# Optimization experiments

Hardware: AMD Instinct MI355X
Metric: run time of the kernel (lower is better)

The kernel has to match this reference:

```python
import jax, jax.numpy as jnp
from jax import lax
import numpy as np

UNITS = 128
IN_DIM = 512
BATCH = 128
SEQ = 1024


def setup_inputs() -> dict:
    key = jax.random.key(0)
    k1, k2, k3 = jax.random.split(key, 3)
    x = jax.random.normal(k1, (BATCH, SEQ, IN_DIM), dtype=jnp.float32)
    # glorot-ish scaling for stability
    W = jax.random.normal(k2, (IN_DIM, 4 * UNITS), dtype=jnp.float32) * (1.0 / np.sqrt(IN_DIM))
    U = jax.random.normal(k3, (UNITS, 4 * UNITS), dtype=jnp.float32) * (1.0 / np.sqrt(UNITS))
    b = jnp.zeros((4 * UNITS,), dtype=jnp.float32)
    return {"x": x, "W": W, "U": U, "b": b}


def reference(x, W, U, b):
    # Keras LSTM with activation='tanh' AND recurrent_activation='tanh'
    # (all four gates use tanh, unlike the standard sigmoid gates).
    # Gate order in Keras kernels: i, f, g(cell candidate), o.
    B = x.shape[0]
    units = U.shape[0]
    # Precompute input projections for all timesteps: [T, B, 4*units]
    xW = jnp.einsum('bti,ij->tbj', x, W) + b

    def step(carry, xw_t):
        h, c = carry
        z = xw_t + h @ U  # [B, 4*units]
        i, f, g, o = jnp.split(z, 4, axis=-1)
        i = jnp.tanh(i)
        f = jnp.tanh(f)
        g = jnp.tanh(g)
        o = jnp.tanh(o)
        c_new = f * c + i * g
        h_new = o * jnp.tanh(c_new)
        return (h_new, c_new), None

    h0 = jnp.zeros((B, units), dtype=x.dtype)
    c0 = jnp.zeros((B, units), dtype=x.dtype)
    (h_last, _), _ = lax.scan(step, (h0, c0), xW)
    return h_last  # [B, units] (return_sequences=False)
```

## Files before the change

### kernel.cpp

```cpp
#include <hip/hip_runtime.h>
#include <hip/hip_bf16.h>


#define UNITS 128
#define IN_DIM 512
#define BATCH 128
#define SEQ 1024
#define GATES 512
#define M_ROWS (BATCH * SEQ)

typedef __attribute__((ext_vector_type(8))) short short8;
typedef __attribute__((ext_vector_type(4))) float floatx4;

__device__ __forceinline__ unsigned short f2bf(float f) {
    unsigned int x = __builtin_bit_cast(unsigned int, f);
    unsigned int r = (x + 0x7fffu + ((x >> 16) & 1u)) >> 16;
    return (unsigned short)r;
}
__device__ __forceinline__ float bf2f(unsigned short u) {
    unsigned int x = ((unsigned int)u) << 16;
    return __builtin_bit_cast(float, x);
}
__device__ __forceinline__ unsigned int pack2(float lo, float hi) {
    return (unsigned int)f2bf(lo) | ((unsigned int)f2bf(hi) << 16);
}

__device__ __forceinline__ float fast_tanh(float x) {
    float xc = fminf(12.0f, fmaxf(-12.0f, x));
    float e = __expf(2.0f * xc);
    return 1.0f - 2.0f * __builtin_amdgcn_rcpf(e + 1.0f);
}

__global__ void k_wt(const float* __restrict__ W, unsigned short* __restrict__ Wt) {
    int idx = blockIdx.x * 256 + threadIdx.x;
    int n = idx >> 9;
    int k = idx & 511;
    Wt[idx] = f2bf(W[k * 512 + n]);
}

template <bool XWF32>
__global__ void __launch_bounds__(256, 2)
k_gemm(const float* __restrict__ A, const unsigned short* __restrict__ Bt,
       void* __restrict__ Cout) {
    __shared__ __align__(16) unsigned short As[128 * 40];
    __shared__ __align__(16) unsigned short Bs[128 * 40];
    const int tid = threadIdx.x;
    const int m0 = blockIdx.y << 7;
    const int n0 = blockIdx.x << 7;
    const int l = tid & 63;
    const int w = tid >> 6;
    const int wr = (w >> 1) << 6;
    const int wc = (w & 1) << 6;
    const int lrow = l & 15;
    const int lq = l >> 4;

    floatx4 acc[4][4] = {};

    const int srow = tid >> 1;
    const int soff = (tid & 1) << 4;
    const float* ap = A + (size_t)(m0 + srow) * 512 + soff;
    const unsigned short* bp = Bt + (size_t)(n0 + srow) * 512 + soff;
    unsigned short* as = &As[srow * 40 + soff];
    unsigned short* bs = &Bs[srow * 40 + soff];

    for (int k0 = 0; k0 < 512; k0 += 32) {
        float4 a0 = *(const float4*)(ap + k0);
        float4 a1 = *(const float4*)(ap + k0 + 4);
        float4 a2 = *(const float4*)(ap + k0 + 8);
        float4 a3 = *(const float4*)(ap + k0 + 12);
        uint4 b0 = *(const uint4*)(bp + k0);
        uint4 b1 = *(const uint4*)(bp + k0 + 8);
        __syncthreads();
        uint4 pa0, pa1;
        pa0.x = pack2(a0.x, a0.y); pa0.y = pack2(a0.z, a0.w);
        pa0.z = pack2(a1.x, a1.y); pa0.w = pack2(a1.z, a1.w);
        pa1.x = pack2(a2.x, a2.y); pa1.y = pack2(a2.z, a2.w);
        pa1.z = pack2(a3.x, a3.y); pa1.w = pack2(a3.z, a3.w);
        *(uint4*)as = pa0;
        *(uint4*)(as + 8) = pa1;
        *(uint4*)bs = b0;
        *(uint4*)(bs + 8) = b1;
        __syncthreads();
        short8 af[4], bfv[4];
#pragma unroll
        for (int mi = 0; mi < 4; ++mi)
            af[mi] = *(const short8*)&As[(wr + mi * 16 + lrow) * 40 + lq * 8];
#pragma unroll
        for (int ni = 0; ni < 4; ++ni)
            bfv[ni] = *(const short8*)&Bs[(wc + ni * 16 + lrow) * 40 + lq * 8];
#pragma unroll
        for (int mi = 0; mi < 4; ++mi)
#pragma unroll
            for (int ni = 0; ni < 4; ++ni)
                acc[mi][ni] = __builtin_amdgcn_mfma_f32_16x16x32_bf16(
                    af[mi], bfv[ni], acc[mi][ni], 0, 0, 0);
    }
#pragma unroll
    for (int mi = 0; mi < 4; ++mi) {
#pragma unroll
        for (int ni = 0; ni < 4; ++ni) {
            int row = m0 + wr + mi * 16 + lq * 4;
            int col = n0 + wc + ni * 16 + lrow;
            if (XWF32) {
                float* Cf = (float*)Cout;
#pragma unroll
                for (int r = 0; r < 4; ++r)
                    Cf[(size_t)(row + r) * 512 + col] = acc[mi][ni][r];
            } else {
                unsigned short* Cb = (unsigned short*)Cout;
#pragma unroll
                for (int r = 0; r < 4; ++r)
                    Cb[(size_t)(row + r) * 512 + col] = f2bf(acc[mi][ni][r]);
            }
        }
    }
}

template <bool XWF32>
__global__ void __launch_bounds__(512, 2)
k_scan(const void* __restrict__ xwv, const float* __restrict__ U,
       const float* __restrict__ bias, float* __restrict__ out) {
    __shared__ __align__(16) float hbuf[2 * 160];
    const int j = threadIdx.x;
    const int bb = blockIdx.x;
    const int m = j >> 2;
    const int r = j & 3;

    float u0[32], u1[32], u2[32], u3[32];
#pragma unroll
    for (int kk = 0; kk < 32; ++kk) {
        const float* Up = U + (size_t)(r * 32 + kk) * 512 + m;
        u0[kk] = Up[0];
        u1[kk] = Up[128];
        u2[kk] = Up[256];
        u3[kk] = Up[384];
    }
    const float bj = bias[r * 128 + m];

    if (j < 160) hbuf[j] = 0.0f;
    __syncthreads();

    const float* xwf = (const float*)xwv + (size_t)bb * SEQ * 512 + r * 128 + m;
    const unsigned short* xwb =
        (const unsigned short*)xwv + (size_t)bb * SEQ * 512 + r * 128 + m;

    float c = 0.0f, hval = 0.0f;
    float xw_cur = XWF32 ? xwf[0] : bf2f(xwb[0]);
    for (int t = 0; t < SEQ; ++t) {
        float xw_next = 0.0f;
        if (t + 1 < SEQ)
            xw_next = XWF32 ? xwf[(size_t)(t + 1) * 512]
                            : bf2f(xwb[(size_t)(t + 1) * 512]);

        const float xb = xw_cur + bj;
        float a0 = (r == 0) ? xb : 0.0f;
        float a1 = (r == 1) ? xb : 0.0f;
        float a2 = (r == 2) ? xb : 0.0f;
        float a3 = (r == 3) ? xb : 0.0f;

        const float4* h4 =
            (const float4*)(hbuf + (t & 1) * 160 + r * 40);
#pragma unroll
        for (int i = 0; i < 8; ++i) {
            float4 hv = h4[i];
            a0 = fmaf(hv.x, u0[4 * i + 0], a0);
            a1 = fmaf(hv.x, u1[4 * i + 0], a1);
            a2 = fmaf(hv.x, u2[4 * i + 0], a2);
            a3 = fmaf(hv.x, u3[4 * i + 0], a3);
            a0 = fmaf(hv.y, u0[4 * i + 1], a0);
            a1 = fmaf(hv.y, u1[4 * i + 1], a1);
            a2 = fmaf(hv.y, u2[4 * i + 1], a2);
            a3 = fmaf(hv.y, u3[4 * i + 1], a3);
            a0 = fmaf(hv.z, u0[4 * i + 2], a0);
            a1 = fmaf(hv.z, u1[4 * i + 2], a1);
            a2 = fmaf(hv.z, u2[4 * i + 2], a2);
            a3 = fmaf(hv.z, u3[4 * i + 2], a3);
            a0 = fmaf(hv.w, u0[4 * i + 3], a0);
            a1 = fmaf(hv.w, u1[4 * i + 3], a1);
            a2 = fmaf(hv.w, u2[4 * i + 3], a2);
            a3 = fmaf(hv.w, u3[4 * i + 3], a3);
        }
        a0 += __shfl_xor(a0, 1);
        a1 += __shfl_xor(a1, 1);
        a2 += __shfl_xor(a2, 1);
        a3 += __shfl_xor(a3, 1);
        a0 += __shfl_xor(a0, 2);
        a1 += __shfl_xor(a1, 2);
        a2 += __shfl_xor(a2, 2);
        a3 += __shfl_xor(a3, 2);

        const float gi = fast_tanh(a0);
        const float gf = fast_tanh(a1);
        const float gg = fast_tanh(a2);
        const float go = fast_tanh(a3);
        c = fmaf(gf, c, gi * gg);
        hval = go * fast_tanh(c);

        if (r == 0)
            hbuf[((t + 1) & 1) * 160 + (m >> 5) * 40 + (m & 31)] = hval;
        __syncthreads();
        xw_cur = xw_next;
    }
    if (r == 0) out[bb * UNITS + m] = hval;
}

extern "C" void kernel_launch(void* const* d_in, const int* in_sizes, int n_in,
                              void* d_out, int out_size, void* d_ws, size_t ws_size,
                              hipStream_t stream) {
    const float* x = (const float*)d_in[0];
    const float* W = (const float*)d_in[1];
    const float* U = (const float*)d_in[2];
    const float* b = (const float*)d_in[3];
    float* out = (float*)d_out;

    char* ws = (char*)d_ws;
    const size_t WT_BYTES = (size_t)512 * 512 * 2;
    unsigned short* Wt = (unsigned short*)ws;
    void* xw = (void*)(ws + WT_BYTES);
    const size_t XW_F32_BYTES = (size_t)M_ROWS * 512 * 4;
    const bool f32path = (ws_size >= WT_BYTES + XW_F32_BYTES);

    k_wt<<<dim3(1024), dim3(256), 0, stream>>>(W, Wt);

    dim3 ggrid(4, 1024);
    if (f32path) {
        k_gemm<true><<<ggrid, dim3(256), 0, stream>>>(x, Wt, xw);
        k_scan<true><<<dim3(128), dim3(512), 0, stream>>>(xw, U, b, out);
    } else {
        k_gemm<false><<<ggrid, dim3(256), 0, stream>>>(x, Wt, xw);
        k_scan<false><<<dim3(128), dim3(512), 0, stream>>>(xw, U, b, out);
    }
}
```

Baseline: 1.217 ms.

## Use packed FMA and DPP transpose-reduce in LSTM recurrent scan

Restructures the per-step recurrent matvec in the scan kernel. It uses v_pk_fma_f32 on paired U weights, and replaces the four xor-shuffle all-reduces with a DPP butterfly transpose-reduce, so each lane computes one gate and needs only one tanh before a DPP broadcast. tanh now uses exp2 directly, and the launch bound drops to one block per SM to give more registers. The aim is to shorten the serial per-timestep critical path, at the cost of inline asm and DPP lane-mapping assumptions.

```diff
diff --git a/kernel.cpp b/kernel.cpp
--- a/kernel.cpp
+++ b/kernel.cpp
@@ -11,6 +11,8 @@
 
 typedef __attribute__((ext_vector_type(8))) short short8;
 typedef __attribute__((ext_vector_type(4))) float floatx4;
+typedef __attribute__((ext_vector_type(4))) float fv4;
+typedef __attribute__((ext_vector_type(2))) float fv2;
 
 __device__ __forceinline__ unsigned short f2bf(float f) {
     unsigned int x = __builtin_bit_cast(unsigned int, f);
@@ -26,9 +28,26 @@
 }
 
 __device__ __forceinline__ float fast_tanh(float x) {
-    float xc = fminf(12.0f, fmaxf(-12.0f, x));
-    float e = __expf(2.0f * xc);
+    float y = fminf(34.6f, fmaxf(-34.6f, x * 2.88539008f));
+    float e = __builtin_amdgcn_exp2f(y);
     return 1.0f - 2.0f * __builtin_amdgcn_rcpf(e + 1.0f);
+}
+
+template <int CTRL>
+__device__ __forceinline__ float dppf(float x) {
+    int xi = __builtin_bit_cast(int, x);
+    int r = __builtin_amdgcn_update_dpp(0, xi, CTRL, 0xF, 0xF, true);
+    return __builtin_bit_cast(float, r);
+}
+#define DPP_XOR1 0xB1
+#define DPP_XOR2 0x4E
+#define DPP_BC0 0x00
+#define DPP_BC1 0x55
+#define DPP_BC2 0xAA
+#define DPP_BC3 0xFF
+
+__device__ __forceinline__ void pk_fma(fv2& acc, fv2 a, fv2 b) {
+    asm("v_pk_fma_f32 %0, %1, %2, %0" : "+v"(acc) : "v"(a), "v"(b));
 }
 
 __global__ void k_wt(const float* __restrict__ W, unsigned short* __restrict__ Wt) {
@@ -117,7 +136,7 @@
 }
 
 template <bool XWF32>
-__global__ void __launch_bounds__(512, 2)
+__global__ void __launch_bounds__(512, 1)
 k_scan(const void* __restrict__ xwv, const float* __restrict__ U,
        const float* __restrict__ bias, float* __restrict__ out) {
     __shared__ __align__(16) float hbuf[2 * 160];
@@ -126,16 +145,19 @@
     const int m = j >> 2;
     const int r = j & 3;
 
-    float u0[32], u1[32], u2[32], u3[32];
-#pragma unroll
-    for (int kk = 0; kk < 32; ++kk) {
-        const float* Up = U + (size_t)(r * 32 + kk) * 512 + m;
-        u0[kk] = Up[0];
-        u1[kk] = Up[128];
-        u2[kk] = Up[256];
-        u3[kk] = Up[384];
+    fv2 u2[4][16];
+#pragma unroll
+    for (int i = 0; i < 16; ++i) {
+        const float* Up0 = U + (size_t)(r * 32 + 2 * i) * 512 + m;
+        const float* Up1 = Up0 + 512;
+        u2[0][i] = (fv2){Up0[0], Up1[0]};
+        u2[1][i] = (fv2){Up0[128], Up1[128]};
+        u2[2][i] = (fv2){Up0[256], Up1[256]};
+        u2[3][i] = (fv2){Up0[384], Up1[384]};
     }
     const float bj = bias[r * 128 + m];
+    const int p = r & 1;
+    const int q = (r >> 1) & 1;
 
     if (j < 160) hbuf[j] = 0.0f;
     __syncthreads();
@@ -145,61 +167,58 @@
         (const unsigned short*)xwv + (size_t)bb * SEQ * 512 + r * 128 + m;
 
     float c = 0.0f, hval = 0.0f;
-    float xw_cur = XWF32 ? xwf[0] : bf2f(xwb[0]);
+    float xb_cur = (XWF32 ? xwf[0] : bf2f(xwb[0])) + bj;
     for (int t = 0; t < SEQ; ++t) {
         float xw_next = 0.0f;
         if (t + 1 < SEQ)
             xw_next = XWF32 ? xwf[(size_t)(t + 1) * 512]
                             : bf2f(xwb[(size_t)(t + 1) * 512]);
 
-        const float xb = xw_cur + bj;
-        float a0 = (r == 0) ? xb : 0.0f;
-        float a1 = (r == 1) ? xb : 0.0f;
-        float a2 = (r == 2) ? xb : 0.0f;
-        float a3 = (r == 3) ? xb : 0.0f;
-
-        const float4* h4 =
-            (const float4*)(hbuf + (t & 1) * 160 + r * 40);
+        fv2 A0 = {0.f, 0.f}, A1 = {0.f, 0.f}, A2 = {0.f, 0.f}, A3 = {0.f, 0.f};
+        const fv4* h4 =
+            (const fv4*)(hbuf + (t & 1) * 160 + r * 40);
 #pragma unroll
         for (int i = 0; i < 8; ++i) {
-            float4 hv = h4[i];
-            a0 = fmaf(hv.x, u0[4 * i + 0], a0);
-            a1 = fmaf(hv.x, u1[4 * i + 0], a1);
-            a2 = fmaf(hv.x, u2[4 * i + 0], a2);
-            a3 = fmaf(hv.x, u3[4 * i + 0], a3);
-            a0 = fmaf(hv.y, u0[4 * i + 1], a0);
-            a1 = fmaf(hv.y, u1[4 * i + 1], a1);
-            a2 = fmaf(hv.y, u2[4 * i + 1], a2);
-            a3 = fmaf(hv.y, u3[4 * i + 1], a3);
-            a0 = fmaf(hv.z, u0[4 * i + 2], a0);
-            a1 = fmaf(hv.z, u1[4 * i + 2], a1);
-            a2 = fmaf(hv.z, u2[4 * i + 2], a2);
-            a3 = fmaf(hv.z, u3[4 * i + 2], a3);
-            a0 = fmaf(hv.w, u0[4 * i + 3], a0);
-            a1 = fmaf(hv.w, u1[4 * i + 3], a1);
-            a2 = fmaf(hv.w, u2[4 * i + 3], a2);
-            a3 = fmaf(hv.w, u3[4 * i + 3], a3);
+            fv4 hv = h4[i];
+            fv2 hl = hv.lo;
+            fv2 hh = hv.hi;
+            pk_fma(A0, hl, u2[0][2 * i]);
+            pk_fma(A1, hl, u2[1][2 * i]);
+            pk_fma(A2, hl, u2[2][2 * i]);
+            pk_fma(A3, hl, u2[3][2 * i]);
+            pk_fma(A0, hh, u2[0][2 * i + 1]);
+            pk_fma(A1, hh, u2[1][2 * i + 1]);
+            pk_fma(A2, hh, u2[2][2 * i + 1]);
+            pk_fma(A3, hh, u2[3][2 * i + 1]);
         }
-        a0 += __shfl_xor(a0, 1);
-        a1 += __shfl_xor(a1, 1);
-        a2 += __shfl_xor(a2, 1);
-        a3 += __shfl_xor(a3, 1);
-        a0 += __shfl_xor(a0, 2);
-        a1 += __shfl_xor(a1, 2);
-        a2 += __shfl_xor(a2, 2);
-        a3 += __shfl_xor(a3, 2);
-
-        const float gi = fast_tanh(a0);
-        const float gf = fast_tanh(a1);
-        const float gg = fast_tanh(a2);
-        const float go = fast_tanh(a3);
+        float s0 = A0.x + A0.y;
+        float s1 = A1.x + A1.y;
+        float s2 = A2.x + A2.y;
+        float s3 = A3.x + A3.y;
+
+        float va = p ? s1 : s0;
+        float oa = p ? s0 : s1;
+        float vb = p ? s3 : s2;
+        float ob = p ? s2 : s3;
+        float a01 = va + dppf<DPP_XOR1>(oa);
+        float a23 = vb + dppf<DPP_XOR1>(ob);
+        float vv = q ? a23 : a01;
+        float oo = q ? a01 : a23;
+        float sigma = vv + dppf<DPP_XOR2>(oo);
+
+        float tg = fast_tanh(sigma + xb_cur);
+
+        float gi = dppf<DPP_BC0>(tg);
+        float gf = dppf<DPP_BC1>(tg);
+        float gg = dppf<DPP_BC2>(tg);
+        float go = dppf<DPP_BC3>(tg);
         c = fmaf(gf, c, gi * gg);
         hval = go * fast_tanh(c);
 
         if (r == 0)
             hbuf[((t + 1) & 1) * 160 + (m >> 5) * 40 + (m & 31)] = hval;
         __syncthreads();
-        xw_cur = xw_next;
+        xb_cur = xw_next + bj;
     }
     if (r == 0) out[bb * UNITS + m] = hval;
 }
```

After: 1.043 ms. 14.3% less time.
